# Performance work log

Measured on AMD Instinct MI355X. Metric: run time of the kernel, lower is better.

Reference implementation:

```python
import jax, jax.numpy as jnp
import numpy as np

B, S = 16, 512
PERC, META = 512, 64
D = PERC + META            # sensory (input) size = 576
UNITS = 512                # ncp_units = hidden_dim * 2
MOTOR = 153                # int(UNITS * 0.3)
HID = 256
HEADS, QTY = 4, 32
HEAD_DIM = HID // HEADS
ODE_UNFOLDS = 6
EPS = 1e-8


def setup_inputs() -> dict:
    key = jax.random.key(0)
    ks = jax.random.split(key, 32)
    u = lambda k, sh, lo, hi: jax.random.uniform(k, sh, jnp.float32, lo, hi)
    n = lambda k, sh, s: jax.random.normal(k, sh, jnp.float32) * jnp.float32(s)
    inp = {}
    inp['x'] = n(ks[0], (B, S, D), 1.0)
    inp['timespans'] = u(ks[1], (B, S), 0.5, 1.5)
    # LTC affine input/output maps
    inp['input_w'] = jnp.ones((D,), jnp.float32)
    inp['input_b'] = jnp.zeros((D,), jnp.float32)
    inp['output_w'] = jnp.ones((MOTOR,), jnp.float32)
    inp['output_b'] = jnp.zeros((MOTOR,), jnp.float32)
    # sensory synapses (ncps init ranges)
    inp['sensory_mu'] = u(ks[2], (D, UNITS), 0.3, 0.8)
    inp['sensory_sigma'] = u(ks[3], (D, UNITS), 3.0, 8.0)
    inp['sensory_w'] = u(ks[4], (D, UNITS), 0.001, 1.0)
    smask = (jax.random.uniform(ks[5], (D, UNITS)) < 0.3).astype(jnp.float32)
    inp['sensory_mask'] = smask
    inp['sensory_erev'] = smask * jnp.sign(jax.random.normal(ks[6], (D, UNITS)))
    # recurrent synapses
    inp['mu'] = u(ks[7], (UNITS, UNITS), 0.3, 0.8)
    inp['sigma'] = u(ks[8], (UNITS, UNITS), 3.0, 8.0)
    inp['w'] = u(ks[9], (UNITS, UNITS), 0.001, 1.0)
    rmask = (jax.random.uniform(ks[10], (UNITS, UNITS)) < 0.3).astype(jnp.float32)
    inp['mask'] = rmask
    inp['erev'] = rmask * jnp.sign(jax.random.normal(ks[11], (UNITS, UNITS)))
    inp['gleak'] = u(ks[12], (UNITS,), 0.001, 1.0)
    inp['vleak'] = u(ks[13], (UNITS,), -0.2, 0.2)
    inp['cm'] = u(ks[14], (UNITS,), 0.4, 0.6)
    # projection 153 -> 256
    inp['proj_W'] = n(ks[15], (MOTOR, HID), 1.0 / np.sqrt(MOTOR))
    inp['proj_b'] = jnp.zeros((HID,), jnp.float32)
    # Hopfield: learned prototypes + q/k/v/out projections
    inp['lookup'] = n(ks[16], (QTY, HID), 1.0 / np.sqrt(HID))
    inp['targets'] = n(ks[17], (QTY, HID), 1.0 / np.sqrt(HID))
    inp['Wq'] = n(ks[18], (HID, HID), 1.0 / np.sqrt(HID))
    inp['Wk'] = n(ks[19], (HID, HID), 1.0 / np.sqrt(HID))
    inp['Wv'] = n(ks[20], (HID, HID), 1.0 / np.sqrt(HID))
    inp['Wo'] = n(ks[21], (HID, HID), 1.0 / np.sqrt(HID))
    inp['bo'] = jnp.zeros((HID,), jnp.float32)
    # belief head 256 -> 256 -> 64
    inp['W1'] = n(ks[22], (HID, HID), 1.0 / np.sqrt(HID))
    inp['b1'] = jnp.zeros((HID,), jnp.float32)
    inp['W2'] = n(ks[23], (HID, 64), 1.0 / np.sqrt(HID))
    inp['b2'] = jnp.zeros((64,), jnp.float32)
    return inp


def _forward(x, timespans, input_w, input_b, sensory_mu, sensory_sigma, sensory_w,
             sensory_erev, sensory_mask, mu, sigma, w, erev, mask, gleak, vleak, cm,
             output_w, output_b, proj_W, proj_b, lookup, targets, Wq, Wk, Wv, Wo, bo,
             W1, b1, W2, b2):
    inp = x * input_w + input_b                       # affine input map (B,S,D)
    sw = jax.nn.softplus(sensory_w)
    wr = jax.nn.softplus(w)
    gl = jax.nn.softplus(gleak)
    cmp = jax.nn.softplus(cm)

    @jax.checkpoint
    def step(v, xs):
        it, el = xs                                   # (B,D), (B,)
        # sensory gating: (B, D, UNITS)
        sact = sw * jax.nn.sigmoid(sensory_sigma * (it[:, :, None] - sensory_mu)) * sensory_mask
        wns = jnp.sum(sact * sensory_erev, axis=1)    # (B, UNITS)
        wds = jnp.sum(sact, axis=1)
        cm_t = cmp / (el[:, None] / ODE_UNFOLDS)      # (B, UNITS)
        for _ in range(ODE_UNFOLDS):
            # recurrent gating: (B, UNITS_pre, UNITS_post)
            wact = wr * jax.nn.sigmoid(sigma * (v[:, :, None] - mu)) * mask
            wn = jnp.sum(wact * erev, axis=1) + wns
            wd = jnp.sum(wact, axis=1) + wds
            v = (cm_t * v + gl * vleak + wn) / (cm_t + gl + wd + EPS)
        y = v[:, :MOTOR] * output_w + output_b        # motor slice + affine output map
        return v, y

    v0 = jnp.zeros((x.shape[0], UNITS), x.dtype)
    vT, ys = jax.lax.scan(step, v0, (jnp.swapaxes(inp, 0, 1), jnp.swapaxes(timespans, 0, 1)))
    ltc_out = jnp.swapaxes(ys, 0, 1)                  # (B, S, MOTOR)

    h = ltc_out @ proj_W + proj_b                     # (B, S, HID)
    # Hopfield associative read: query=h, keys/values=learned prototypes
    q = (h @ Wq).reshape(h.shape[0], h.shape[1], HEADS, HEAD_DIM)
    k = (lookup @ Wk).reshape(QTY, HEADS, HEAD_DIM)
    val = (targets @ Wv).reshape(QTY, HEADS, HEAD_DIM)
    scores = jnp.einsum('bshd,qhd->bshq', q, k) / np.float32(np.sqrt(HEAD_DIM))
    attn = jax.nn.softmax(scores, axis=-1)
    mem = jnp.einsum('bshq,qhd->bshd', attn, val).reshape(h.shape[0], h.shape[1], HID) @ Wo + bo

    combined = h + mem
    belief = jax.nn.silu(combined @ W1 + b1) @ W2 + b2
    return combined, belief, vT


def reference(x, timespans, input_w, input_b, sensory_mu, sensory_sigma, sensory_w,
              sensory_erev, sensory_mask, mu, sigma, w, erev, mask, gleak, vleak, cm,
              output_w, output_b, proj_W, proj_b, lookup, targets, Wq, Wk, Wv, Wo, bo,
              W1, b1, W2, b2):
    return _forward(x, timespans, input_w, input_b, sensory_mu, sensory_sigma, sensory_w,
                    sensory_erev, sensory_mask, mu, sigma, w, erev, mask, gleak, vleak, cm,
                    output_w, output_b, proj_W, proj_b, lookup, targets, Wq, Wk, Wv, Wo, bo,
                    W1, b1, W2, b2)
```

## Files before the change

### kernel.cpp

```cpp
#include <hip/hip_runtime.h>
#include <hip/hip_bf16.h>
#include <math.h>


#define B_     16
#define S_     512
#define D_     576
#define U_     512
#define MOTOR_ 153
#define HID_   256
#define QTY_   32
#define STRIDE 240
#define LOG2E  1.4426950408889634f
#define SPIN_MAX (1 << 22)

#if __has_builtin(__builtin_amdgcn_exp2f)
#define EXP2F(x) __builtin_amdgcn_exp2f(x)
#else
#define EXP2F(x) exp2f(x)
#endif
#if __has_builtin(__builtin_amdgcn_rcpf)
#define RCPF(x) __builtin_amdgcn_rcpf(x)
#else
#define RCPF(x) (1.0f/(x))
#endif
#if __has_builtin(__builtin_amdgcn_s_sleep)
#define SLEEP1() __builtin_amdgcn_s_sleep(1)
#else
#define SLEEP1()
#endif

__device__ __forceinline__ float rcp_nr(float x) {
  float r = RCPF(x);
  return r * (2.0f - x * r);
}

__device__ __forceinline__ float softplusf(float x) {
  return (x > 20.0f) ? x : log1pf(expf(x));
}

extern "C" __global__ __launch_bounds__(512)
void k_build(const float* __restrict__ smu, const float* __restrict__ ssig,
             const float* __restrict__ sw,  const float* __restrict__ smask,
             const float* __restrict__ serev,
             const float* __restrict__ rmu, const float* __restrict__ rsig,
             const float* __restrict__ rw,  const float* __restrict__ rmask,
             const float* __restrict__ rerev,
             const float* __restrict__ gleak, const float* __restrict__ vleak,
             const float* __restrict__ cm,
             float4* __restrict__ recW, float4* __restrict__ senW,
             int* __restrict__ recNit, int* __restrict__ senNit,
             float* __restrict__ glA, float* __restrict__ glvA,
             float* __restrict__ cmA, int* __restrict__ gflag,
             unsigned long long* __restrict__ vG)
{
  const int j = threadIdx.x;
  if (blockIdx.x == 0) {
    float gl = softplusf(gleak[j]);
    glA[j] = gl; glvA[j] = gl * vleak[j];
    cmA[j] = softplusf(cm[j]);
    if (j == 0) gflag[0] = 0;
    #pragma unroll
    for (int t = 0; t < 32; ++t) vG[j + 512*t] = 0ull;
    int cnt = 0;
    for (int i = 0; i < U_; ++i) {
      float mk = rmask[i*U_ + j];
      if (mk != 0.0f) {
        float A  = rsig[i*U_ + j] * LOG2E;
        float Bc = A * rmu[i*U_ + j];
        float Wm = softplusf(rw[i*U_ + j]) * mk;
        float er = rerev[i*U_ + j];
        unsigned code = (er > 0.f) ? 1u : ((er < 0.f) ? 2u : 0u);
        if (cnt < STRIDE)
          recW[j*STRIDE + cnt] = make_float4(A, Bc, Wm,
                                 __uint_as_float((unsigned)i | (code << 12)));
        ++cnt;
      }
    }
    if (cnt > STRIDE) cnt = STRIDE;
    int padded = (cnt + 15) & ~15;
    for (int t = cnt; t < padded; ++t)
      recW[j*STRIDE + t] = make_float4(0.f, 0.f, 0.f, __uint_as_float(0u));
    recNit[j] = padded >> 4;
  } else {
    int cnt = 0;
    for (int i = 0; i < D_; ++i) {
      float mk = smask[i*U_ + j];
      if (mk != 0.0f) {
        float A  = ssig[i*U_ + j] * LOG2E;
        float Bc = A * smu[i*U_ + j];
        float Wm = softplusf(sw[i*U_ + j]) * mk;
        float er = serev[i*U_ + j];
        unsigned code = (er > 0.f) ? 1u : ((er < 0.f) ? 2u : 0u);
        if (cnt < STRIDE)
          senW[j*STRIDE + cnt] = make_float4(A, Bc, Wm,
                                 __uint_as_float((unsigned)i | (code << 12)));
        ++cnt;
      }
    }
    if (cnt > STRIDE) cnt = STRIDE;
    int padded = (cnt + 15) & ~15;
    for (int t = cnt; t < padded; ++t)
      senW[j*STRIDE + t] = make_float4(0.f, 0.f, 0.f, __uint_as_float(0u));
    senNit[j] = padded >> 3;
  }
}

extern "C" __global__ __launch_bounds__(256)
void k_sens(const float* __restrict__ x, const float* __restrict__ iw,
            const float* __restrict__ ib,
            const float4* __restrict__ senW, const int* __restrict__ senNit,
            float* __restrict__ sensN, float* __restrict__ sensD)
{
  __shared__ float4 wl[32*STRIDE];
  __shared__ float  itl[D_];
  const int chunk = blockIdx.x & 15;
  const int slice = blockIdx.x >> 4;
  const int tid = threadIdx.x;
  for (int t = tid; t < 32*STRIDE; t += 256) wl[t] = senW[chunk*32*STRIDE + t];
  const int cl = tid >> 3, part = tid & 7;
  const int col = chunk*32 + cl;
  const int nIt = senNit[col];
  const int base = cl*STRIDE;
  __syncthreads();
  for (int pr = slice*64; pr < slice*64 + 64; ++pr) {
    for (int t = tid; t < D_; t += 256) itl[t] = x[pr*D_ + t]*iw[t] + ib[t];
    __syncthreads();
    float an = 0.f, ad = 0.f;
    for (int it = 0; it < nIt; ++it) {
      float4 w4 = wl[base + it*8 + part];
      unsigned meta = __float_as_uint(w4.w);
      float vv = itl[meta & 1023u];
      float e = EXP2F(w4.y - w4.x * vv);
      float r = rcp_nr(1.0f + e);
      ad += w4.z * r;
      unsigned code = meta >> 12;
      float we = (code == 1u) ? w4.z : ((code == 2u) ? -w4.z : 0.0f);
      an += we * r;
    }
    an += __shfl_xor(an, 1); an += __shfl_xor(an, 2); an += __shfl_xor(an, 4);
    ad += __shfl_xor(ad, 1); ad += __shfl_xor(ad, 2); ad += __shfl_xor(ad, 4);
    if (part == 0) { sensN[pr*U_ + col] = an; sensD[pr*U_ + col] = ad; }
    __syncthreads();
  }
}

extern "C" __global__ __launch_bounds__(512)
void k_scan(const float* __restrict__ ts,
            const float4* __restrict__ recW, const int* __restrict__ recNit,
            const float* __restrict__ glA, const float* __restrict__ glvA,
            const float* __restrict__ cmA,
            const float* __restrict__ sensN, const float* __restrict__ sensD,
            const float* __restrict__ ow, const float* __restrict__ ob,
            float* __restrict__ ltc, int* gflag, unsigned long long* vG,
            float* __restrict__ vT_out)
{
  __shared__ float4 wl[32*STRIDE];
  __shared__ float  vl[2][U_];
  const int bid = blockIdx.x;
  const int batch = (bid & 7) + ((bid >> 7) << 3);
  const int chunk = (bid >> 3) & 15;
  const int tid = threadIdx.x;
  for (int t = tid; t < 32*STRIDE; t += 512) wl[t] = recW[chunk*32*STRIDE + t];
  const int cl = tid >> 4, part = tid & 15;
  const int col = chunk*32 + cl;
  const int nIt = recNit[col];
  const int base = cl*STRIDE;
  float gl = 0.f, glv = 0.f, cmsp = 0.f;
  if (part == 0) { gl = glA[col]; glv = glvA[col]; cmsp = cmA[col]; }
  vl[0][tid] = 0.0f;
  unsigned long long* vg0 = vG + batch*U_;
  unsigned long long* vg1 = vG + 16*U_ + batch*U_;
  float sn = 0.f, sd = 0.f, cmt = 0.f;
  if (part == 0) {
    float el = ts[batch*S_];
    sn = sensN[batch*S_*U_ + col];
    sd = sensD[batch*S_*U_ + col];
    cmt = cmsp / (el / 6.0f);
  }
  __syncthreads();
  int p = 0, cur = 0;
  for (int s = 0; s < S_; ++s) {
    float snN = 0.f, sdN = 0.f, elN = 0.f;
    for (int u = 0; u < 6; ++u, ++p) {
      const float* vc = vl[cur];
      float wn = 0.f, wd = 0.f;
      for (int it = 0; it < nIt; ++it) {
        float4 w4 = wl[base + it*16 + part];
        unsigned meta = __float_as_uint(w4.w);
        float vv = vc[meta & 1023u];
        float e = EXP2F(w4.y - w4.x * vv);
        float r = rcp_nr(1.0f + e);
        wd += w4.z * r;
        unsigned code = meta >> 12;
        float we = (code == 1u) ? w4.z : ((code == 2u) ? -w4.z : 0.0f);
        wn += we * r;
      }
      if (u == 0 && part == 0) {
        int s2 = (s + 1 < S_) ? (s + 1) : (S_ - 1);
        elN = ts[batch*S_ + s2];
        snN = sensN[(batch*S_ + s2)*U_ + col];
        sdN = sensD[(batch*S_ + s2)*U_ + col];
      }
      wn += __shfl_xor(wn, 1); wd += __shfl_xor(wd, 1);
      wn += __shfl_xor(wn, 2); wd += __shfl_xor(wd, 2);
      wn += __shfl_xor(wn, 4); wd += __shfl_xor(wd, 4);
      wn += __shfl_xor(wn, 8); wd += __shfl_xor(wd, 8);
      unsigned long long* vg = (p & 1) ? vg1 : vg0;
      if (part == 0) {
        float vold = vc[col];
        float num = cmt*vold + glv + wn + sn;
        float den = cmt + gl + wd + sd + 1e-8f;
        float vnew = num / den;
        unsigned long long pk =
            ((unsigned long long)(unsigned)(p + 1) << 32) |
            (unsigned long long)__float_as_uint(vnew);
        __hip_atomic_store(&vg[col], pk, __ATOMIC_RELAXED,
                           __HIP_MEMORY_SCOPE_AGENT);
      }
      {
        const unsigned need = (unsigned)(p + 1);
        unsigned long long pk;
        int itc = 0;
        for (;;) {
          pk = __hip_atomic_load(&vg[tid], __ATOMIC_RELAXED,
                                 __HIP_MEMORY_SCOPE_AGENT);
          if ((unsigned)(pk >> 32) >= need) break;
          ++itc;
          if ((itc & 4095) == 0) {
            if (itc >= SPIN_MAX ||
                __hip_atomic_load(gflag, __ATOMIC_RELAXED,
                                  __HIP_MEMORY_SCOPE_AGENT) != 0) {
              __hip_atomic_store(gflag, 1, __ATOMIC_RELAXED,
                                 __HIP_MEMORY_SCOPE_AGENT);
              break;
            }
          }
          SLEEP1();
        }
        vl[cur ^ 1][tid] = __uint_as_float((unsigned)pk);
      }
      __syncthreads();
      cur ^= 1;
    }
    if (part == 0) {
      sn = snN; sd = sdN; cmt = cmsp / (elN / 6.0f);
    }
    if (chunk == 0) {
      for (int m = tid; m < MOTOR_; m += 512)
        ltc[(batch*S_ + s)*MOTOR_ + m] = vl[cur][m]*ow[m] + ob[m];
    }
  }
  if (chunk == 0) vT_out[batch*U_ + tid] = vl[cur][tid];
}

extern "C" __global__ __launch_bounds__(256)
void k_proj(const float* __restrict__ ltc, const float* __restrict__ pW,
            const float* __restrict__ pb, float* __restrict__ hbuf)
{
  __shared__ float lr[16*MOTOR_];
  const int rb = blockIdx.x * 16;
  const int tid = threadIdx.x;
  for (int t = tid; t < 16*MOTOR_; t += 256) lr[t] = ltc[rb*MOTOR_ + t];
  __syncthreads();
  float acc[16];
  #pragma unroll
  for (int r = 0; r < 16; ++r) acc[r] = 0.f;
  for (int i = 0; i < MOTOR_; ++i) {
    float wv = pW[i*HID_ + tid];
    #pragma unroll
    for (int r = 0; r < 16; ++r) acc[r] += lr[r*MOTOR_ + i] * wv;
  }
  float bb = pb[tid];
  #pragma unroll
  for (int r = 0; r < 16; ++r) hbuf[(rb + r)*HID_ + tid] = acc[r] + bb;
}

extern "C" __global__ __launch_bounds__(256)
void k_kv(const float* __restrict__ lookup, const float* __restrict__ targets,
          const float* __restrict__ Wk, const float* __restrict__ Wv,
          float* __restrict__ khvh)
{
  __shared__ float src[HID_];
  const int mat = blockIdx.x >> 5, pp = blockIdx.x & 31;
  const int tid = threadIdx.x;
  src[tid] = (mat ? targets : lookup)[pp*HID_ + tid];
  __syncthreads();
  const float* W = mat ? Wv : Wk;
  float a = 0.f;
  for (int i = 0; i < HID_; ++i) a += src[i] * W[i*HID_ + tid];
  khvh[mat*QTY_*HID_ + pp*HID_ + tid] = a;
}

extern "C" __global__ __launch_bounds__(256)
void k_hop(const float* __restrict__ hbuf, const float* __restrict__ Wq,
           const float* __restrict__ khvh, const float* __restrict__ Wo,
           const float* __restrict__ bo, float* __restrict__ outC)
{
  __shared__ float hr[16][HID_];
  __shared__ float qr[16][HID_];
  __shared__ float sc[QTY_][65];
  __shared__ float mr[16][HID_];
  const int rb = blockIdx.x * 16;
  const int tid = threadIdx.x;
  for (int t = tid; t < 16*HID_; t += 256) (&hr[0][0])[t] = hbuf[rb*HID_ + t];
  __syncthreads();
  {
    float acc[16];
    #pragma unroll
    for (int r = 0; r < 16; ++r) acc[r] = 0.f;
    for (int i = 0; i < HID_; ++i) {
      float wv = Wq[i*HID_ + tid];
      #pragma unroll
      for (int r = 0; r < 16; ++r) acc[r] += hr[r][i] * wv;
    }
    #pragma unroll
    for (int r = 0; r < 16; ++r) qr[r][tid] = acc[r];
  }
  __syncthreads();
  if (tid < 128) {
    const int pp = tid >> 2, hh = tid & 3;
    const float* kp = khvh + pp*HID_ + hh*64;
    for (int row = 0; row < 16; ++row) {
      float sacc = 0.f;
      for (int d = 0; d < 64; ++d) sacc += qr[row][hh*64 + d] * kp[d];
      sc[pp][row*4 + hh] = sacc * 0.125f;
    }
  }
  __syncthreads();
  if (tid < 64) {
    const int c = tid;
    float mx = -1e30f;
    for (int pp = 0; pp < QTY_; ++pp) mx = fmaxf(mx, sc[pp][c]);
    float sum = 0.f;
    for (int pp = 0; pp < QTY_; ++pp) {
      float e = expf(sc[pp][c] - mx); sc[pp][c] = e; sum += e;
    }
    float inv = 1.f/sum;
    for (int pp = 0; pp < QTY_; ++pp) sc[pp][c] *= inv;
  }
  __syncthreads();
  {
    const int hh = tid >> 6;
    float acc[16];
    #pragma unroll
    for (int r = 0; r < 16; ++r) acc[r] = 0.f;
    for (int pp = 0; pp < QTY_; ++pp) {
      float vv = khvh[QTY_*HID_ + pp*HID_ + tid];
      #pragma unroll
      for (int r = 0; r < 16; ++r) acc[r] += sc[pp][r*4 + hh] * vv;
    }
    #pragma unroll
    for (int r = 0; r < 16; ++r) mr[r][tid] = acc[r];
  }
  __syncthreads();
  {
    float acc[16];
    #pragma unroll
    for (int r = 0; r < 16; ++r) acc[r] = 0.f;
    for (int i = 0; i < HID_; ++i) {
      float wv = Wo[i*HID_ + tid];
      #pragma unroll
      for (int r = 0; r < 16; ++r) acc[r] += mr[r][i] * wv;
    }
    float bb = bo[tid];
    #pragma unroll
    for (int r = 0; r < 16; ++r)
      outC[(rb + r)*HID_ + tid] = hr[r][tid] + acc[r] + bb;
  }
}

extern "C" __global__ __launch_bounds__(256)
void k_belief(const float* __restrict__ outC, const float* __restrict__ W1,
              const float* __restrict__ b1, const float* __restrict__ W2,
              const float* __restrict__ b2, float* __restrict__ outB)
{
  __shared__ float cr[16][HID_];
  __shared__ float trr[16][HID_];
  const int rb = blockIdx.x * 16;
  const int tid = threadIdx.x;
  for (int t = tid; t < 16*HID_; t += 256) (&cr[0][0])[t] = outC[rb*HID_ + t];
  __syncthreads();
  {
    float acc[16];
    #pragma unroll
    for (int r = 0; r < 16; ++r) acc[r] = 0.f;
    for (int i = 0; i < HID_; ++i) {
      float wv = W1[i*HID_ + tid];
      #pragma unroll
      for (int r = 0; r < 16; ++r) acc[r] += cr[r][i] * wv;
    }
    float bb = b1[tid];
    #pragma unroll
    for (int r = 0; r < 16; ++r) {
      float xx = acc[r] + bb;
      trr[r][tid] = xx / (1.0f + expf(-xx));
    }
  }
  __syncthreads();
  {
    const int o = tid & 63, rr = tid >> 6;
    float a4[4] = {0.f, 0.f, 0.f, 0.f};
    for (int i = 0; i < HID_; ++i) {
      float wv = W2[i*64 + o];
      a4[0] += trr[rr    ][i] * wv;
      a4[1] += trr[rr + 4][i] * wv;
      a4[2] += trr[rr + 8][i] * wv;
      a4[3] += trr[rr +12][i] * wv;
    }
    float bb = b2[o];
    outB[(rb + rr     )*64 + o] = a4[0] + bb;
    outB[(rb + rr + 4 )*64 + o] = a4[1] + bb;
    outB[(rb + rr + 8 )*64 + o] = a4[2] + bb;
    outB[(rb + rr + 12)*64 + o] = a4[3] + bb;
  }
}

extern "C" void kernel_launch(void* const* d_in, const int* in_sizes, int n_in,
                              void* d_out, int out_size, void* d_ws,
                              size_t ws_size, hipStream_t stream)
{
  const float* x       = (const float*)d_in[0];
  const float* ts      = (const float*)d_in[1];
  const float* iw      = (const float*)d_in[2];
  const float* ib      = (const float*)d_in[3];
  const float* ow      = (const float*)d_in[4];
  const float* ob      = (const float*)d_in[5];
  const float* smu     = (const float*)d_in[6];
  const float* ssig    = (const float*)d_in[7];
  const float* sw      = (const float*)d_in[8];
  const float* smask   = (const float*)d_in[9];
  const float* serev   = (const float*)d_in[10];
  const float* rmu     = (const float*)d_in[11];
  const float* rsig    = (const float*)d_in[12];
  const float* rw      = (const float*)d_in[13];
  const float* rmask   = (const float*)d_in[14];
  const float* rerev   = (const float*)d_in[15];
  const float* gleak   = (const float*)d_in[16];
  const float* vleak   = (const float*)d_in[17];
  const float* cm      = (const float*)d_in[18];
  const float* pW      = (const float*)d_in[19];
  const float* pb      = (const float*)d_in[20];
  const float* lookup  = (const float*)d_in[21];
  const float* targets = (const float*)d_in[22];
  const float* Wq      = (const float*)d_in[23];
  const float* Wk      = (const float*)d_in[24];
  const float* Wv      = (const float*)d_in[25];
  const float* Wo      = (const float*)d_in[26];
  const float* bo      = (const float*)d_in[27];
  const float* W1      = (const float*)d_in[28];
  const float* b1      = (const float*)d_in[29];
  const float* W2      = (const float*)d_in[30];
  const float* b2      = (const float*)d_in[31];

  float4* recW  = (float4*)d_ws;
  float4* senW  = recW + 512*STRIDE;
  int*    recNit = (int*)(senW + 512*STRIDE);
  int*    senNit = recNit + 512;
  float*  glA   = (float*)(senNit + 512);
  float*  glvA  = glA + 512;
  float*  cmA   = glvA + 512;
  int*    gflag = (int*)(cmA + 512);
  unsigned long long* vG = (unsigned long long*)(gflag + 128);
  float*  sensN = (float*)(vG + 2*16*U_);
  float*  sensD = sensN + B_*S_*U_;
  float*  ltc   = sensD + B_*S_*U_;
  float*  hbuf  = ltc + B_*S_*MOTOR_;
  float*  khvh  = hbuf + B_*S_*HID_;

  float* outC = (float*)d_out;
  float* outB = outC + B_*S_*HID_;
  float* outV = outB + B_*S_*64;

  k_build<<<dim3(2), dim3(512), 0, stream>>>(
      smu, ssig, sw, smask, serev, rmu, rsig, rw, rmask, rerev,
      gleak, vleak, cm, recW, senW, recNit, senNit, glA, glvA, cmA,
      gflag, vG);
  k_sens<<<dim3(2048), dim3(256), 0, stream>>>(
      x, iw, ib, senW, senNit, sensN, sensD);
  k_scan<<<dim3(256), dim3(512), 0, stream>>>(
      ts, recW, recNit, glA, glvA, cmA, sensN, sensD, ow, ob,
      ltc, gflag, vG, outV);
  k_proj<<<dim3(512), dim3(256), 0, stream>>>(ltc, pW, pb, hbuf);
  k_kv<<<dim3(64), dim3(256), 0, stream>>>(lookup, targets, Wk, Wv, khvh);
  k_hop<<<dim3(512), dim3(256), 0, stream>>>(hbuf, Wq, khvh, Wo, bo, outC);
  k_belief<<<dim3(512), dim3(256), 0, stream>>>(outC, W1, b1, W2, b2, outB);
}
```

Measured before the change: 11.91 ms.

## Funnel cross-block state exchange through one wave and distribute motor writes

In the recurrent scan, each block now stages its 32 new voltages in shared memory and a single wave publishes them and polls peers' flagged values. Each lane batch-loads 8 entries per round without sleeping, replacing 512 threads that each spun with sleeps. Motor output and final-state writes are spread across chunks instead of done by chunk 0 alone. The sensory kernel uses half as many blocks, each covering 128 rows, which reduces redundant weight loads into shared memory. The tradeoff is an extra barrier per unfold, polling that stays busy, and less parallelism in the sensory kernel.

Result: no change. 11.90 ms (-0.1%).

```diff
diff --git a/kernel.cpp b/kernel.cpp
--- a/kernel.cpp
+++ b/kernel.cpp
@@ -12,7 +12,7 @@
 #define QTY_   32
 #define STRIDE 240
 #define LOG2E  1.4426950408889634f
-#define SPIN_MAX (1 << 22)
+#define SPIN_ROUNDS (1 << 20)
 
 #if __has_builtin(__builtin_amdgcn_exp2f)
 #define EXP2F(x) __builtin_amdgcn_exp2f(x)
@@ -23,11 +23,6 @@
 #define RCPF(x) __builtin_amdgcn_rcpf(x)
 #else
 #define RCPF(x) (1.0f/(x))
-#endif
-#if __has_builtin(__builtin_amdgcn_s_sleep)
-#define SLEEP1() __builtin_amdgcn_s_sleep(1)
-#else
-#define SLEEP1()
 #endif
 
 __device__ __forceinline__ float rcp_nr(float x) {
@@ -114,8 +109,8 @@
 {
   __shared__ float4 wl[32*STRIDE];
   __shared__ float  itl[D_];
-  const int chunk = blockIdx.x & 15;
-  const int slice = blockIdx.x >> 4;
+  const int chunk = blockIdx.x >> 6;
+  const int slice = blockIdx.x & 63;
   const int tid = threadIdx.x;
   for (int t = tid; t < 32*STRIDE; t += 256) wl[t] = senW[chunk*32*STRIDE + t];
   const int cl = tid >> 3, part = tid & 7;
@@ -123,7 +118,7 @@
   const int nIt = senNit[col];
   const int base = cl*STRIDE;
   __syncthreads();
-  for (int pr = slice*64; pr < slice*64 + 64; ++pr) {
+  for (int pr = slice*128; pr < slice*128 + 128; ++pr) {
     for (int t = tid; t < D_; t += 256) itl[t] = x[pr*D_ + t]*iw[t] + ib[t];
     __syncthreads();
     float an = 0.f, ad = 0.f;
@@ -157,6 +152,7 @@
 {
   __shared__ float4 wl[32*STRIDE];
   __shared__ float  vl[2][U_];
+  __shared__ unsigned long long pkStage[32];
   const int bid = blockIdx.x;
   const int batch = (bid & 7) + ((bid >> 7) << 3);
   const int chunk = (bid >> 3) & 15;
@@ -166,6 +162,12 @@
   const int col = chunk*32 + cl;
   const int nIt = recNit[col];
   const int base = cl*STRIDE;
+  const int wave = tid >> 6, lane = tid & 63;
+  const bool ownLane = (lane >= 4*chunk) && (lane < 4*chunk + 4);
+  const int mcol = chunk*32 + (tid & 31);
+  const bool mWrite = (tid < 32) && (mcol < MOTOR_);
+  float mow = 0.f, mob = 0.f;
+  if (mWrite) { mow = ow[mcol]; mob = ob[mcol]; }
   float gl = 0.f, glv = 0.f, cmsp = 0.f;
   if (part == 0) { gl = glA[col]; glv = glvA[col]; cmsp = cmA[col]; }
   vl[0][tid] = 0.0f;
@@ -184,6 +186,7 @@
     float snN = 0.f, sdN = 0.f, elN = 0.f;
     for (int u = 0; u < 6; ++u, ++p) {
       const float* vc = vl[cur];
+      float* vlN = vl[cur ^ 1];
       float wn = 0.f, wd = 0.f;
       for (int it = 0; it < nIt; ++it) {
         float4 w4 = wl[base + it*16 + part];
@@ -207,28 +210,39 @@
       wn += __shfl_xor(wn, 4); wd += __shfl_xor(wd, 4);
       wn += __shfl_xor(wn, 8); wd += __shfl_xor(wd, 8);
       unsigned long long* vg = (p & 1) ? vg1 : vg0;
+      const unsigned need = (unsigned)(p + 1);
       if (part == 0) {
         float vold = vc[col];
         float num = cmt*vold + glv + wn + sn;
         float den = cmt + gl + wd + sd + 1e-8f;
         float vnew = num / den;
-        unsigned long long pk =
-            ((unsigned long long)(unsigned)(p + 1) << 32) |
-            (unsigned long long)__float_as_uint(vnew);
-        __hip_atomic_store(&vg[col], pk, __ATOMIC_RELAXED,
-                           __HIP_MEMORY_SCOPE_AGENT);
-      }
-      {
-        const unsigned need = (unsigned)(p + 1);
-        unsigned long long pk;
-        int itc = 0;
-        for (;;) {
-          pk = __hip_atomic_load(&vg[tid], __ATOMIC_RELAXED,
-                                 __HIP_MEMORY_SCOPE_AGENT);
-          if ((unsigned)(pk >> 32) >= need) break;
-          ++itc;
-          if ((itc & 4095) == 0) {
-            if (itc >= SPIN_MAX ||
+        vlN[col] = vnew;
+        pkStage[cl] = ((unsigned long long)need << 32) |
+                      (unsigned long long)__float_as_uint(vnew);
+      }
+      __syncthreads();
+      if (wave == 0) {
+        if (lane < 32) {
+          __hip_atomic_store(&vg[chunk*32 + lane], pkStage[lane],
+                             __ATOMIC_RELAXED, __HIP_MEMORY_SCOPE_AGENT);
+        }
+        unsigned pend = ownLane ? 0u : 0xFFu;
+        int rounds = 0;
+        while (pend) {
+          unsigned long long t[8];
+          #pragma unroll
+          for (int j = 0; j < 8; ++j)
+            if (pend & (1u << j))
+              t[j] = __hip_atomic_load(&vg[8*lane + j], __ATOMIC_RELAXED,
+                                       __HIP_MEMORY_SCOPE_AGENT);
+          #pragma unroll
+          for (int j = 0; j < 8; ++j)
+            if ((pend & (1u << j)) && (unsigned)(t[j] >> 32) >= need) {
+              vlN[8*lane + j] = __uint_as_float((unsigned)t[j]);
+              pend &= ~(1u << j);
+            }
+          if ((++rounds & 63) == 0) {
+            if (rounds >= SPIN_ROUNDS ||
                 __hip_atomic_load(gflag, __ATOMIC_RELAXED,
                                   __HIP_MEMORY_SCOPE_AGENT) != 0) {
               __hip_atomic_store(gflag, 1, __ATOMIC_RELAXED,
@@ -236,9 +250,7 @@
               break;
             }
           }
-          SLEEP1();
         }
-        vl[cur ^ 1][tid] = __uint_as_float((unsigned)pk);
       }
       __syncthreads();
       cur ^= 1;
@@ -246,12 +258,11 @@
     if (part == 0) {
       sn = snN; sd = sdN; cmt = cmsp / (elN / 6.0f);
     }
-    if (chunk == 0) {
-      for (int m = tid; m < MOTOR_; m += 512)
-        ltc[(batch*S_ + s)*MOTOR_ + m] = vl[cur][m]*ow[m] + ob[m];
-    }
-  }
-  if (chunk == 0) vT_out[batch*U_ + tid] = vl[cur][tid];
+    if (mWrite)
+      ltc[(batch*S_ + s)*MOTOR_ + mcol] = vl[cur][mcol]*mow + mob;
+  }
+  if (tid < 32)
+    vT_out[batch*U_ + chunk*32 + tid] = vl[cur][chunk*32 + tid];
 }
 
 extern "C" __global__ __launch_bounds__(256)
@@ -476,7 +487,7 @@
       smu, ssig, sw, smask, serev, rmu, rsig, rw, rmask, rerev,
       gleak, vleak, cm, recW, senW, recNit, senNit, glA, glvA, cmA,
       gflag, vG);
-  k_sens<<<dim3(2048), dim3(256), 0, stream>>>(
+  k_sens<<<dim3(1024), dim3(256), 0, stream>>>(
       x, iw, ib, senW, senNit, sensN, sensD);
   k_scan<<<dim3(256), dim3(512), 0, stream>>>(
       ts, recW, recNit, glA, glvA, cmA, sensN, sensD, ow, ob,
```
